# Kernel tuning notes

Measured on AMD Instinct MI355X. Metric: run time of the kernel, lower is better.

The kernel has to match this reference:

```python
import jax, jax.numpy as jnp
import numpy as np

ALPHA = 0.2  # LeakyReLU negative slope


def setup_inputs() -> dict:
    key = jax.random.key(0)
    k1, k2, k3, k4 = jax.random.split(key, 4)
    B, N, IN_F, OUT_F = 8, 2048, 128, 64
    inputs = jax.random.normal(k1, (B, N, IN_F), dtype=jnp.float32)
    nodes_embedding = jax.random.normal(k2, (B, N, OUT_F), dtype=jnp.float32)
    # xavier-uniform-like init (gain 1.414)
    limW = 1.414 * np.sqrt(6.0 / (IN_F + OUT_F))
    W = jax.random.uniform(k3, (IN_F, OUT_F), dtype=jnp.float32, minval=-limW, maxval=limW)
    lima = 1.414 * np.sqrt(6.0 / (4 * OUT_F + 1))
    a = jax.random.uniform(k4, (4 * OUT_F, 1), dtype=jnp.float32, minval=-lima, maxval=lima)
    return {"inputs": inputs, "nodes_embedding": nodes_embedding, "W": W, "a": a}


def reference(inputs, nodes_embedding, W, a):
    # x_w: [B,N,F]
    x_w = jnp.matmul(inputs, W)
    # h: [B,N,2F]
    h = jnp.concatenate([nodes_embedding, x_w], axis=2)
    twoF = h.shape[-1]
    # Separable form of concat-based attention: a_input[b,i,j] = [h_i, h_j],
    # so a_input @ a = (h_i . a1) + (h_j . a2). Avoids the O(B*N^2*4F) tensor.
    a1 = a[:twoF, 0]  # [2F]
    a2 = a[twoF:, 0]  # [2F]
    s1 = jnp.einsum('bnf,f->bn', h, a1)  # [B,N]
    s2 = jnp.einsum('bnf,f->bn', h, a2)  # [B,N]
    e = jax.nn.leaky_relu(s1[:, :, None] + s2[:, None, :], negative_slope=ALPHA)  # [B,N,N]
    attention = jax.nn.softmax(e, axis=2)  # softmax over j
    # dropout: eval mode (training=False) -> identity
    h_prime = jnp.matmul(attention, x_w)  # [B,N,F]
    return (jax.nn.relu(h_prime), attention)
```

## Files before the change

kernel.cpp:

```cpp
#include <hip/hip_runtime.h>

#define ALPHA 0.2f
#define B_    8
#define N_    2048
#define INF_  128
#define OUTF_ 64

typedef __attribute__((ext_vector_type(8))) short short8;
typedef __attribute__((ext_vector_type(4))) float f32x4;

__device__ __forceinline__ unsigned short f2bf(float f) {
    unsigned int x = __float_as_uint(f);
    return (unsigned short)((x + 0x7fffu + ((x >> 16) & 1u)) >> 16);
}

__global__ __launch_bounds__(256) void prep_kernel(
    const float* __restrict__ inp,
    const float* __restrict__ nodes,
    const float* __restrict__ Wm,
    const float* __restrict__ av,
    unsigned short* __restrict__ xwT,
    float* __restrict__ s1_out,
    float* __restrict__ s2_out)
{
    __shared__ float w_lds[INF_ * OUTF_];
    __shared__ float in_lds[16 * INF_];
    __shared__ __align__(16) unsigned short t_lds[64 * 16];
    const int tid  = threadIdx.x;
    const int wave = tid >> 6, lane = tid & 63;
    const int r0   = blockIdx.x * 16;

    {
        const float4* Wv = (const float4*)Wm;
        float4* wd = (float4*)w_lds;
        #pragma unroll
        for (int q = 0; q < 8; q++) wd[tid + q * 256] = Wv[tid + q * 256];
        const float4* Iv = (const float4*)(inp + (size_t)r0 * INF_);
        float4* id4 = (float4*)in_lds;
        id4[tid]       = Iv[tid];
        id4[tid + 256] = Iv[tid + 256];
    }
    __syncthreads();

    float acc[4] = {0.f, 0.f, 0.f, 0.f};
    const float* inw = &in_lds[(wave * 4) * INF_];
    #pragma unroll 4
    for (int k = 0; k < INF_; k++) {
        float wv = w_lds[k * OUTF_ + lane];
        acc[0] += inw[k]            * wv;
        acc[1] += inw[INF_ + k]     * wv;
        acc[2] += inw[2 * INF_ + k] * wv;
        acc[3] += inw[3 * INF_ + k] * wv;
    }

    const float a1n = av[lane];
    const float a1x = av[64 + lane];
    const float a2n = av[128 + lane];
    const float a2x = av[192 + lane];

    #pragma unroll
    for (int rr = 0; rr < 4; rr++) {
        const int row = r0 + wave * 4 + rr;
        float nf = nodes[(size_t)row * OUTF_ + lane];
        float p1 = nf * a1n + acc[rr] * a1x;
        float p2 = nf * a2n + acc[rr] * a2x;
        #pragma unroll
        for (int off = 32; off; off >>= 1) {
            p1 += __shfl_down(p1, off);
            p2 += __shfl_down(p2, off);
        }
        if (lane == 0) { s1_out[row] = p1; s2_out[row] = p2; }
        t_lds[lane * 16 + wave * 4 + rr] = f2bf(acc[rr]);
    }
    __syncthreads();

    {
        const int n  = tid >> 2, c0 = (tid & 3) * 4;
        const int b  = r0 >> 11, rb = r0 & (N_ - 1);
        *(uint2*)(xwT + ((size_t)b * OUTF_ + n) * N_ + rb + c0) =
            *(const uint2*)&t_lds[n * 16 + c0];
    }
}

__global__ __launch_bounds__(256) void attn_kernel(
    const unsigned short* __restrict__ xwT,
    const float* __restrict__ s1g,
    const float* __restrict__ s2g,
    float* __restrict__ out_h,
    float* __restrict__ out_att)
{
    __shared__ float s2_lds[N_];
    __shared__ float s1_lds[64];
    __shared__ float m_lds[64];
    __shared__ float li_lds[64];
    __shared__ float redmax[4];

    const int tid  = threadIdx.x;
    const int wave = tid >> 6, lane = tid & 63;
    const int b  = blockIdx.x >> 5;
    const int i0 = (blockIdx.x & 31) << 6;

    {
        const float4* s2v = (const float4*)(s2g + b * N_);
        float4* d4 = (float4*)s2_lds;
        d4[tid]       = s2v[tid];
        d4[tid + 256] = s2v[tid + 256];
    }
    if (tid < 64) s1_lds[tid] = s1g[b * N_ + i0 + tid];
    __syncthreads();

    {
        float lm = -1e30f;
        for (int idx = tid; idx < N_; idx += 256) lm = fmaxf(lm, s2_lds[idx]);
        #pragma unroll
        for (int off = 32; off; off >>= 1) lm = fmaxf(lm, __shfl_xor(lm, off));
        if (lane == 0) redmax[wave] = lm;
    }
    __syncthreads();
    const float s2max = fmaxf(fmaxf(redmax[0], redmax[1]),
                              fmaxf(redmax[2], redmax[3]));

    {
        const int i = tid >> 2, jo = tid & 3;
        const float s1v = s1_lds[i];
        const float vm = s1v + s2max;
        const float m = vm > 0.f ? vm : ALPHA * vm;
        float l = 0.f;
        for (int j4 = jo * 4; j4 < N_; j4 += 16) {
            float4 s = *(const float4*)&s2_lds[j4];
            float v0 = s1v + s.x, v1 = s1v + s.y, v2 = s1v + s.z, v3 = s1v + s.w;
            l += __expf(fmaxf(v0, ALPHA * v0) - m);
            l += __expf(fmaxf(v1, ALPHA * v1) - m);
            l += __expf(fmaxf(v2, ALPHA * v2) - m);
            l += __expf(fmaxf(v3, ALPHA * v3) - m);
        }
        l += __shfl_xor(l, 1);
        l += __shfl_xor(l, 2);
        if (jo == 0) { m_lds[i] = m; li_lds[i] = 1.f / l; }
    }
    __syncthreads();

    const int row16 = lane & 15;
    const int quad  = lane >> 4;
    const int irow  = wave * 16 + row16;
    const float s1v = s1_lds[irow];
    const float mr  = m_lds[irow];
    const float lir = li_lds[irow];

    const unsigned short* bptr[4];
    #pragma unroll
    for (int g = 0; g < 4; g++)
        bptr[g] = xwT + ((size_t)b * OUTF_ + g * 16 + row16) * N_ + quad * 8;

    float* attp = out_att + ((size_t)(b * N_ + i0 + irow)) * N_ + quad * 8;
    const float* s2q = s2_lds + quad * 8;

    f32x4 acc0 = {0.f,0.f,0.f,0.f}, acc1 = {0.f,0.f,0.f,0.f};
    f32x4 acc2 = {0.f,0.f,0.f,0.f}, acc3 = {0.f,0.f,0.f,0.f};

    uint4 bnext[4];
    #pragma unroll
    for (int g = 0; g < 4; g++) bnext[g] = *(const uint4*)bptr[g];

    for (int jt = 0; jt < N_; jt += 32) {
        uint4 bc0 = bnext[0], bc1 = bnext[1], bc2 = bnext[2], bc3 = bnext[3];
        const int jn = (jt + 32) & (N_ - 1);
        #pragma unroll
        for (int g = 0; g < 4; g++) bnext[g] = *(const uint4*)(bptr[g] + jn);

        float4 sa = *(const float4*)(s2q + jt);
        float4 sb = *(const float4*)(s2q + jt + 4);
        float av8[8];
        {
            float v;
            v = s1v + sa.x; av8[0] = __expf(fmaxf(v, ALPHA * v) - mr) * lir;
            v = s1v + sa.y; av8[1] = __expf(fmaxf(v, ALPHA * v) - mr) * lir;
            v = s1v + sa.z; av8[2] = __expf(fmaxf(v, ALPHA * v) - mr) * lir;
            v = s1v + sa.w; av8[3] = __expf(fmaxf(v, ALPHA * v) - mr) * lir;
            v = s1v + sb.x; av8[4] = __expf(fmaxf(v, ALPHA * v) - mr) * lir;
            v = s1v + sb.y; av8[5] = __expf(fmaxf(v, ALPHA * v) - mr) * lir;
            v = s1v + sb.z; av8[6] = __expf(fmaxf(v, ALPHA * v) - mr) * lir;
            v = s1v + sb.w; av8[7] = __expf(fmaxf(v, ALPHA * v) - mr) * lir;
        }
        *(float4*)(attp + jt)     = make_float4(av8[0], av8[1], av8[2], av8[3]);
        *(float4*)(attp + jt + 4) = make_float4(av8[4], av8[5], av8[6], av8[7]);

        short8 a8;
        #pragma unroll
        for (int jj = 0; jj < 8; jj++) a8[jj] = (short)f2bf(av8[jj]);

        acc0 = __builtin_amdgcn_mfma_f32_16x16x32_bf16(a8, *(short8*)&bc0, acc0, 0, 0, 0);
        acc1 = __builtin_amdgcn_mfma_f32_16x16x32_bf16(a8, *(short8*)&bc1, acc1, 0, 0, 0);
        acc2 = __builtin_amdgcn_mfma_f32_16x16x32_bf16(a8, *(short8*)&bc2, acc2, 0, 0, 0);
        acc3 = __builtin_amdgcn_mfma_f32_16x16x32_bf16(a8, *(short8*)&bc3, acc3, 0, 0, 0);
    }

    {
        const size_t hb = ((size_t)(b * N_) + i0 + wave * 16) * OUTF_;
        #pragma unroll
        for (int r = 0; r < 4; r++) {
            const size_t ro = hb + (size_t)(quad * 4 + r) * OUTF_ + row16;
            out_h[ro]      = fmaxf(acc0[r], 0.f);
            out_h[ro + 16] = fmaxf(acc1[r], 0.f);
            out_h[ro + 32] = fmaxf(acc2[r], 0.f);
            out_h[ro + 48] = fmaxf(acc3[r], 0.f);
        }
    }
}

extern "C" void kernel_launch(void* const* d_in, const int* in_sizes, int n_in,
                              void* d_out, int out_size, void* d_ws, size_t ws_size,
                              hipStream_t stream) {
    const float* inp   = (const float*)d_in[0];
    const float* nodes = (const float*)d_in[1];
    const float* Wm    = (const float*)d_in[2];
    const float* av    = (const float*)d_in[3];

    float* out_h   = (float*)d_out;
    float* out_att = out_h + (size_t)B_ * N_ * OUTF_;

    unsigned short* xwT = (unsigned short*)d_ws;
    float* s1_ws = (float*)((char*)d_ws + (size_t)B_ * OUTF_ * N_ * sizeof(unsigned short));
    float* s2_ws = s1_ws + (size_t)B_ * N_;

    prep_kernel<<<(B_ * N_) / 16, 256, 0, stream>>>(inp, nodes, Wm, av,
                                                    xwT, s1_ws, s2_ws);
    attn_kernel<<<(B_ * N_) / 64, 256, 0, stream>>>(xwT, s1_ws, s2_ws,
                                                    out_h, out_att);
}
```

Before: 192.9 us.

## Split j-range across waves, use exp2 with folded softmax constants, nontemporal stores

The attention kernel now uses 512-thread blocks in which two wave groups each process half of the j range, and their MFMA partial sums are reduced through LDS. Softmax is rewritten with exp2 and precomputed log2e-scaled s2 tables for both LeakyReLU branches, with the row max and log-sum folded into per-row constants so each element needs one exp and no multiply. Attention and h outputs use nontemporal stores, and blocks interleave batches. The prep kernel handles 32 rows per block and reads inputs directly from global memory instead of staging them in LDS.

```diff
diff --git a/kernel.cpp b/kernel.cpp
--- a/kernel.cpp
+++ b/kernel.cpp
@@ -5,6 +5,7 @@
 #define N_    2048
 #define INF_  128
 #define OUTF_ 64
+#define LOG2E 1.4426950408889634f
 
 typedef __attribute__((ext_vector_type(8))) short short8;
 typedef __attribute__((ext_vector_type(4))) float f32x4;
@@ -24,34 +25,37 @@
     float* __restrict__ s2_out)
 {
     __shared__ float w_lds[INF_ * OUTF_];
-    __shared__ float in_lds[16 * INF_];
-    __shared__ __align__(16) unsigned short t_lds[64 * 16];
+    __shared__ __align__(16) unsigned short t_lds[64 * 40];
     const int tid  = threadIdx.x;
     const int wave = tid >> 6, lane = tid & 63;
-    const int r0   = blockIdx.x * 16;
+    const int r0   = blockIdx.x * 32;
 
     {
         const float4* Wv = (const float4*)Wm;
         float4* wd = (float4*)w_lds;
         #pragma unroll
         for (int q = 0; q < 8; q++) wd[tid + q * 256] = Wv[tid + q * 256];
-        const float4* Iv = (const float4*)(inp + (size_t)r0 * INF_);
-        float4* id4 = (float4*)in_lds;
-        id4[tid]       = Iv[tid];
-        id4[tid + 256] = Iv[tid + 256];
-    }
-    __syncthreads();
-
-    float acc[4] = {0.f, 0.f, 0.f, 0.f};
-    const float* inw = &in_lds[(wave * 4) * INF_];
+    }
+    __syncthreads();
+
+    const int wv = __builtin_amdgcn_readfirstlane(wave);
+    const float* __restrict__ rbase = inp + (size_t)(r0 + wv * 8) * INF_;
+
+    float acc0[8] = {0.f,0.f,0.f,0.f,0.f,0.f,0.f,0.f};
+    float acc1[8] = {0.f,0.f,0.f,0.f,0.f,0.f,0.f,0.f};
     #pragma unroll 4
-    for (int k = 0; k < INF_; k++) {
-        float wv = w_lds[k * OUTF_ + lane];
-        acc[0] += inw[k]            * wv;
-        acc[1] += inw[INF_ + k]     * wv;
-        acc[2] += inw[2 * INF_ + k] * wv;
-        acc[3] += inw[3 * INF_ + k] * wv;
-    }
+    for (int k = 0; k < INF_; k += 2) {
+        const float w0 = w_lds[k * OUTF_ + lane];
+        const float w1 = w_lds[(k + 1) * OUTF_ + lane];
+        #pragma unroll
+        for (int rr = 0; rr < 8; rr++) {
+            acc0[rr] += rbase[rr * INF_ + k]     * w0;
+            acc1[rr] += rbase[rr * INF_ + k + 1] * w1;
+        }
+    }
+    float acc[8];
+    #pragma unroll
+    for (int rr = 0; rr < 8; rr++) acc[rr] = acc0[rr] + acc1[rr];
 
     const float a1n = av[lane];
     const float a1x = av[64 + lane];
@@ -59,8 +63,8 @@
     const float a2x = av[192 + lane];
 
     #pragma unroll
-    for (int rr = 0; rr < 4; rr++) {
-        const int row = r0 + wave * 4 + rr;
+    for (int rr = 0; rr < 8; rr++) {
+        const int row = r0 + wv * 8 + rr;
         float nf = nodes[(size_t)row * OUTF_ + lane];
         float p1 = nf * a1n + acc[rr] * a1x;
         float p2 = nf * a2n + acc[rr] * a2x;
@@ -70,90 +74,100 @@
             p2 += __shfl_down(p2, off);
         }
         if (lane == 0) { s1_out[row] = p1; s2_out[row] = p2; }
-        t_lds[lane * 16 + wave * 4 + rr] = f2bf(acc[rr]);
-    }
-    __syncthreads();
-
-    {
-        const int n  = tid >> 2, c0 = (tid & 3) * 4;
-        const int b  = r0 >> 11, rb = r0 & (N_ - 1);
-        *(uint2*)(xwT + ((size_t)b * OUTF_ + n) * N_ + rb + c0) =
-            *(const uint2*)&t_lds[n * 16 + c0];
-    }
-}
-
-__global__ __launch_bounds__(256) void attn_kernel(
+        t_lds[lane * 40 + wv * 8 + rr] = f2bf(acc[rr]);
+    }
+    __syncthreads();
+
+    {
+        const int f = tid >> 2, g = tid & 3;
+        const int b = r0 >> 11, rb = r0 & (N_ - 1);
+        *(uint4*)(xwT + ((size_t)b * OUTF_ + f) * N_ + rb + g * 8) =
+            *(const uint4*)&t_lds[f * 40 + g * 8];
+    }
+}
+
+__global__ __launch_bounds__(512, 2) void attn_kernel(
     const unsigned short* __restrict__ xwT,
     const float* __restrict__ s1g,
     const float* __restrict__ s2g,
     float* __restrict__ out_h,
     float* __restrict__ out_att)
 {
-    __shared__ float s2_lds[N_];
+    __shared__ float s2L[N_];
+    __shared__ float s2A[N_];
     __shared__ float s1_lds[64];
-    __shared__ float m_lds[64];
-    __shared__ float li_lds[64];
-    __shared__ float redmax[4];
+    __shared__ float c1_lds[64];
+    __shared__ float c2_lds[64];
+    __shared__ float redmax[8];
+    __shared__ f32x4 redacc[4][64][4];
 
     const int tid  = threadIdx.x;
     const int wave = tid >> 6, lane = tid & 63;
-    const int b  = blockIdx.x >> 5;
-    const int i0 = (blockIdx.x & 31) << 6;
-
-    {
-        const float4* s2v = (const float4*)(s2g + b * N_);
-        float4* d4 = (float4*)s2_lds;
-        d4[tid]       = s2v[tid];
-        d4[tid + 256] = s2v[tid + 256];
-    }
-    if (tid < 64) s1_lds[tid] = s1g[b * N_ + i0 + tid];
-    __syncthreads();
-
-    {
-        float lm = -1e30f;
-        for (int idx = tid; idx < N_; idx += 256) lm = fmaxf(lm, s2_lds[idx]);
+    const int b  = blockIdx.x & 7;
+    const int i0 = (blockIdx.x >> 3) << 6;
+
+    {
+        float4 v = *(const float4*)(s2g + b * N_ + tid * 4);
+        float lm = fmaxf(fmaxf(v.x, v.y), fmaxf(v.z, v.w));
+        *(float4*)&s2L[tid * 4] = make_float4(v.x * LOG2E, v.y * LOG2E,
+                                              v.z * LOG2E, v.w * LOG2E);
+        *(float4*)&s2A[tid * 4] = make_float4(v.x * (ALPHA * LOG2E), v.y * (ALPHA * LOG2E),
+                                              v.z * (ALPHA * LOG2E), v.w * (ALPHA * LOG2E));
         #pragma unroll
         for (int off = 32; off; off >>= 1) lm = fmaxf(lm, __shfl_xor(lm, off));
         if (lane == 0) redmax[wave] = lm;
     }
-    __syncthreads();
-    const float s2max = fmaxf(fmaxf(redmax[0], redmax[1]),
-                              fmaxf(redmax[2], redmax[3]));
-
-    {
-        const int i = tid >> 2, jo = tid & 3;
-        const float s1v = s1_lds[i];
-        const float vm = s1v + s2max;
-        const float m = vm > 0.f ? vm : ALPHA * vm;
+    if (tid < 64) s1_lds[tid] = s1g[b * N_ + i0 + tid];
+    __syncthreads();
+
+    float s2max = redmax[0];
+    #pragma unroll
+    for (int w = 1; w < 8; w++) s2max = fmaxf(s2max, redmax[w]);
+
+    {
+        const int row = tid >> 3, jo = tid & 7;
+        const float s1v = s1_lds[row];
+        const float vm  = s1v + s2max;
+        const float mL  = (vm > 0.f ? vm : ALPHA * vm) * LOG2E;
+        const float d1  = s1v * LOG2E - mL;
+        const float d2  = s1v * (ALPHA * LOG2E) - mL;
         float l = 0.f;
-        for (int j4 = jo * 4; j4 < N_; j4 += 16) {
-            float4 s = *(const float4*)&s2_lds[j4];
-            float v0 = s1v + s.x, v1 = s1v + s.y, v2 = s1v + s.z, v3 = s1v + s.w;
-            l += __expf(fmaxf(v0, ALPHA * v0) - m);
-            l += __expf(fmaxf(v1, ALPHA * v1) - m);
-            l += __expf(fmaxf(v2, ALPHA * v2) - m);
-            l += __expf(fmaxf(v3, ALPHA * v3) - m);
+        for (int j = jo * 4; j < N_; j += 32) {
+            float4 xl = *(const float4*)&s2L[j];
+            float4 xa = *(const float4*)&s2A[j];
+            l += __builtin_amdgcn_exp2f(fmaxf(d1 + xl.x, d2 + xa.x));
+            l += __builtin_amdgcn_exp2f(fmaxf(d1 + xl.y, d2 + xa.y));
+            l += __builtin_amdgcn_exp2f(fmaxf(d1 + xl.z, d2 + xa.z));
+            l += __builtin_amdgcn_exp2f(fmaxf(d1 + xl.w, d2 + xa.w));
         }
         l += __shfl_xor(l, 1);
         l += __shfl_xor(l, 2);
-        if (jo == 0) { m_lds[i] = m; li_lds[i] = 1.f / l; }
+        l += __shfl_xor(l, 4);
+        if (jo == 0) {
+            const float lg = __builtin_amdgcn_logf(l);
+            c1_lds[row] = d1 - lg;
+            c2_lds[row] = d2 - lg;
+        }
     }
     __syncthreads();
 
     const int row16 = lane & 15;
     const int quad  = lane >> 4;
-    const int irow  = wave * 16 + row16;
-    const float s1v = s1_lds[irow];
-    const float mr  = m_lds[irow];
-    const float lir = li_lds[irow];
+    const int wsub  = wave & 3;
+    const int jh    = wave >> 2;
+    const int irow  = wsub * 16 + row16;
+    const float c1  = c1_lds[irow];
+    const float c2  = c2_lds[irow];
+    const int jb    = jh * 1024;
 
     const unsigned short* bptr[4];
     #pragma unroll
     for (int g = 0; g < 4; g++)
-        bptr[g] = xwT + ((size_t)b * OUTF_ + g * 16 + row16) * N_ + quad * 8;
-
-    float* attp = out_att + ((size_t)(b * N_ + i0 + irow)) * N_ + quad * 8;
-    const float* s2q = s2_lds + quad * 8;
+        bptr[g] = xwT + ((size_t)b * OUTF_ + g * 16 + row16) * N_ + jb + quad * 8;
+
+    float* attp = out_att + ((size_t)(b * N_ + i0 + irow)) * N_ + jb + quad * 8;
+    const float* pL = s2L + jb + quad * 8;
+    const float* pA = s2A + jb + quad * 8;
 
     f32x4 acc0 = {0.f,0.f,0.f,0.f}, acc1 = {0.f,0.f,0.f,0.f};
     f32x4 acc2 = {0.f,0.f,0.f,0.f}, acc3 = {0.f,0.f,0.f,0.f};
@@ -162,28 +176,30 @@
     #pragma unroll
     for (int g = 0; g < 4; g++) bnext[g] = *(const uint4*)bptr[g];
 
-    for (int jt = 0; jt < N_; jt += 32) {
+    for (int jt = 0; jt < 1024; jt += 32) {
         uint4 bc0 = bnext[0], bc1 = bnext[1], bc2 = bnext[2], bc3 = bnext[3];
-        const int jn = (jt + 32) & (N_ - 1);
+        const int jn = (jt + 32) & 1023;
         #pragma unroll
         for (int g = 0; g < 4; g++) bnext[g] = *(const uint4*)(bptr[g] + jn);
 
-        float4 sa = *(const float4*)(s2q + jt);
-        float4 sb = *(const float4*)(s2q + jt + 4);
+        float4 sa = *(const float4*)(pL + jt);
+        float4 sb = *(const float4*)(pL + jt + 4);
+        float4 ta = *(const float4*)(pA + jt);
+        float4 tb = *(const float4*)(pA + jt + 4);
         float av8[8];
-        {
-            float v;
-            v = s1v + sa.x; av8[0] = __expf(fmaxf(v, ALPHA * v) - mr) * lir;
-            v = s1v + sa.y; av8[1] = __expf(fmaxf(v, ALPHA * v) - mr) * lir;
-            v = s1v + sa.z; av8[2] = __expf(fmaxf(v, ALPHA * v) - mr) * lir;
-            v = s1v + sa.w; av8[3] = __expf(fmaxf(v, ALPHA * v) - mr) * lir;
-            v = s1v + sb.x; av8[4] = __expf(fmaxf(v, ALPHA * v) - mr) * lir;
-            v = s1v + sb.y; av8[5] = __expf(fmaxf(v, ALPHA * v) - mr) * lir;
-            v = s1v + sb.z; av8[6] = __expf(fmaxf(v, ALPHA * v) - mr) * lir;
-            v = s1v + sb.w; av8[7] = __expf(fmaxf(v, ALPHA * v) - mr) * lir;
-        }
-        *(float4*)(attp + jt)     = make_float4(av8[0], av8[1], av8[2], av8[3]);
-        *(float4*)(attp + jt + 4) = make_float4(av8[4], av8[5], av8[6], av8[7]);
+        av8[0] = __builtin_amdgcn_exp2f(fmaxf(c1 + sa.x, c2 + ta.x));
+        av8[1] = __builtin_amdgcn_exp2f(fmaxf(c1 + sa.y, c2 + ta.y));
+        av8[2] = __builtin_amdgcn_exp2f(fmaxf(c1 + sa.z, c2 + ta.z));
+        av8[3] = __builtin_amdgcn_exp2f(fmaxf(c1 + sa.w, c2 + ta.w));
+        av8[4] = __builtin_amdgcn_exp2f(fmaxf(c1 + sb.x, c2 + tb.x));
+        av8[5] = __builtin_amdgcn_exp2f(fmaxf(c1 + sb.y, c2 + tb.y));
+        av8[6] = __builtin_amdgcn_exp2f(fmaxf(c1 + sb.z, c2 + tb.z));
+        av8[7] = __builtin_amdgcn_exp2f(fmaxf(c1 + sb.w, c2 + tb.w));
+
+        f32x4 o0 = {av8[0], av8[1], av8[2], av8[3]};
+        f32x4 o1 = {av8[4], av8[5], av8[6], av8[7]};
+        __builtin_nontemporal_store(o0, (f32x4*)(attp + jt));
+        __builtin_nontemporal_store(o1, (f32x4*)(attp + jt + 4));
 
         short8 a8;
         #pragma unroll
@@ -195,15 +211,26 @@
         acc3 = __builtin_amdgcn_mfma_f32_16x16x32_bf16(a8, *(short8*)&bc3, acc3, 0, 0, 0);
     }
 
-    {
-        const size_t hb = ((size_t)(b * N_) + i0 + wave * 16) * OUTF_;
+    if (wave >= 4) {
+        redacc[wsub][lane][0] = acc0;
+        redacc[wsub][lane][1] = acc1;
+        redacc[wsub][lane][2] = acc2;
+        redacc[wsub][lane][3] = acc3;
+    }
+    __syncthreads();
+    if (wave < 4) {
+        acc0 += redacc[wsub][lane][0];
+        acc1 += redacc[wsub][lane][1];
+        acc2 += redacc[wsub][lane][2];
+        acc3 += redacc[wsub][lane][3];
+        const size_t hb = ((size_t)(b * N_) + i0 + wsub * 16) * OUTF_;
         #pragma unroll
         for (int r = 0; r < 4; r++) {
             const size_t ro = hb + (size_t)(quad * 4 + r) * OUTF_ + row16;
-            out_h[ro]      = fmaxf(acc0[r], 0.f);
-            out_h[ro + 16] = fmaxf(acc1[r], 0.f);
-            out_h[ro + 32] = fmaxf(acc2[r], 0.f);
-            out_h[ro + 48] = fmaxf(acc3[r], 0.f);
+            __builtin_nontemporal_store(fmaxf(acc0[r], 0.f), out_h + ro);
+            __builtin_nontemporal_store(fmaxf(acc1[r], 0.f), out_h + ro + 16);
+            __builtin_nontemporal_store(fmaxf(acc2[r], 0.f), out_h + ro + 32);
+            __builtin_nontemporal_store(fmaxf(acc3[r], 0.f), out_h + ro + 48);
         }
     }
 }
@@ -223,8 +250,7 @@
     float* s1_ws = (float*)((char*)d_ws + (size_t)B_ * OUTF_ * N_ * sizeof(unsigned short));
     float* s2_ws = s1_ws + (size_t)B_ * N_;
 
-    prep_kernel<<<(B_ * N_) / 16, 256, 0, stream>>>(inp, nodes, Wm, av,
+    prep_kernel<<<(B_ * N_) / 32, 256, 0, stream>>>(inp, nodes, Wm, av,
                                                     xwT, s1_ws, s2_ws);
-    attn_kernel<<<(B_ * N_) / 64, 256, 0, stream>>>(xwT, s1_ws, s2_ws,
-                                                    out_h, out_att);
-}
+    attn_kernel<<<256, 512, 0, stream>>>(xwT, s1_ws, s2_ws, out_h, out_att);
+}
```

After: 226.2 us. +17.2%, slower.
